# Optimization experiments

Measured on AMD Instinct MI355X. Metric: run time of the kernel, lower is better.

The kernel has to match this reference:

```python
import jax, jax.numpy as jnp
import numpy as np
import itertools

B, K, H, W = 64, 5, 320, 320
EPS = 1e-6
# All K! permutations (exact equivalent of scipy.linear_sum_assignment for KxK cost)
PERMS = np.array(list(itertools.permutations(range(K))), dtype=np.int32)  # [P, K]


def setup_inputs() -> dict:
    key = jax.random.key(0)
    k1, k2, k3 = jax.random.split(key, 3)
    return {
        "fg_logits": jax.random.normal(k1, (B, 1, H, W), dtype=jnp.float32),
        "slot_logits": jax.random.normal(k2, (B, K, H, W), dtype=jnp.float32),
        "target": jax.random.uniform(k3, (B, 1, H, W), dtype=jnp.float32),
    }


def reference(fg_logits, slot_logits, target):
    fg = target[:, 0]            # [B,H,W]
    bg = 1.0 - fg                # [B,H,W]
    # targets_b: index 0 = FG mask, 1..K-1 = BG mask (duplicated)  -> [B,K,H,W]
    targets = jnp.concatenate([fg[:, None], jnp.broadcast_to(bg[:, None], (B, K - 1, H, W))], axis=1)

    # IoU cost matrix on detached sigmoid probs (matches .detach())
    probs = jax.lax.stop_gradient(jax.nn.sigmoid(slot_logits))
    s = probs.reshape(B, K, -1)        # [B,K,N]
    t = targets.reshape(B, K, -1)      # [B,K,N]
    inter = jnp.einsum('bkn,bjn->bkj', s, t)           # [B,K,K]
    union = s.sum(-1)[:, :, None] + t.sum(-1)[:, None, :] - inter + EPS
    cost = 1.0 - inter / union                          # [B,K,K]

    # Exact Hungarian via brute force over K! permutations (K small)
    perms = jnp.asarray(PERMS)                          # [P,K]
    rows = jnp.arange(K)[None, :]                       # [1,K]
    perm_cost = cost[:, rows, perms].sum(-1)            # [B,P]
    best_perm = perms[jnp.argmin(perm_cost, axis=1)]    # [B,K] col_ind per sample

    # aligned[i] = targets[col_ind[i]]; targets[j] is fg iff j == 0
    is_fg = (best_perm == 0)[:, :, None, None]          # [B,K,1,1]
    aligned = jnp.where(is_fg, fg[:, None], bg[:, None])  # [B,K,H,W]

    # Stable sigmoid-BCE with logits, mean-reduced per sample then averaged over B
    x = slot_logits
    bce = jnp.maximum(x, 0.0) - x * aligned + jnp.log1p(jnp.exp(-jnp.abs(x)))
    return bce.mean()
```

## Files before the change

kernel.cpp:

```cpp
#include <hip/hip_runtime.h>


#define BB 64
#define KK 5
#define NPIX 102400
#define QUARTERS 4
#define SEG 25600
#define ITERS 25
#define THREADS 256
#define REC 8
#define NBLK (BB * KK * QUARTERS)

typedef float v4f __attribute__((ext_vector_type(4)));

__global__ void hung_pass1(const float* __restrict__ slot,
                           const float* __restrict__ tgt,
                           float* __restrict__ ws)
{
    const int bid = blockIdx.x;
    const int vid = (bid & 7) * (NBLK / 8) + (bid >> 3);
    const int q   = vid & (QUARTERS - 1);
    const int bk  = vid >> 2;
    const int b   = bk / KK;

    const float* xk = slot + (size_t)bk * NPIX + q * SEG;
    const float* t  = tgt  + (size_t)b  * NPIX + q * SEG;

    float X = 0.f, XF = 0.f, S = 0.f, SF = 0.f, PX = 0.f, Tf = 0.f;

    const int base = threadIdx.x * 4;
    #pragma unroll 5
    for (int i = 0; i < ITERS; ++i) {
        const int off = base + i * (THREADS * 4);
        const v4f fg4 = *reinterpret_cast<const v4f*>(t  + off);
        const v4f x4  = *reinterpret_cast<const v4f*>(xk + off);
        #pragma unroll
        for (int u = 0; u < 4; ++u) {
            const float x  = x4[u];
            const float fg = fg4[u];
            const float e  = __expf(-fabsf(x));
            const float qq = 1.0f + e;
            const float r  = __builtin_amdgcn_rcpf(qq);
            const float d  = __logf(qq) + fmaxf(-x, 0.0f);
            const float s  = (x >= 0.0f) ? r : e * r;
            PX += d;
            X  += x;
            XF  = fmaf(x, fg, XF);
            S  += s;
            SF  = fmaf(s, fg, SF);
            Tf += fg;
        }
    }

    float v[6] = {X, XF, S, SF, PX, Tf};
    #pragma unroll
    for (int j = 0; j < 6; ++j) {
        float x = v[j];
        #pragma unroll
        for (int off = 32; off > 0; off >>= 1) x += __shfl_down(x, off, 64);
        v[j] = x;
    }
    __shared__ float red[THREADS / 64][6];
    const int lane = threadIdx.x & 63;
    const int w    = threadIdx.x >> 6;
    if (lane == 0) {
        #pragma unroll
        for (int j = 0; j < 6; ++j) red[w][j] = v[j];
    }
    __syncthreads();
    if (threadIdx.x < 6) {
        const int j = threadIdx.x;
        ws[(size_t)vid * REC + j] =
            red[0][j] + red[1][j] + red[2][j] + red[3][j];
    }
}

__global__ __launch_bounds__(320) void hung_pass2(const float* __restrict__ ws,
                                                  float* __restrict__ out)
{
    __shared__ float red[BB][KK][6];
    const int t = threadIdx.x;
    if (t < BB * KK) {
        float v[6] = {0, 0, 0, 0, 0, 0};
        #pragma unroll
        for (int q = 0; q < QUARTERS; ++q) {
            const float* p = ws + (size_t)(t * QUARTERS + q) * REC;
            #pragma unroll
            for (int j = 0; j < 6; ++j) v[j] += p[j];
        }
        const int b = t / KK, k = t - b * KK;
        #pragma unroll
        for (int j = 0; j < 6; ++j) red[b][k][j] = v[j];
    }
    __syncthreads();
    if (t < BB) {
        const int b = t;
        const float Tf = red[b][0][5];
        const float Tb = (float)NPIX - Tf;
        float best = 3.402823466e+38f; int kb = 0;
        float xfsum = 0.f, px = 0.f;
        #pragma unroll
        for (int k = 0; k < KK; ++k) {
            const float Sv = red[b][k][2], Iv = red[b][k][3];
            const float cf = 1.f - Iv / (Sv + Tf - Iv + 1e-6f);
            const float Ib = Sv - Iv;
            const float cb = 1.f - Ib / (Sv + Tb - Ib + 1e-6f);
            const float dd = cf - cb;
            if (dd < best) { best = dd; kb = k; }
            xfsum += red[b][k][1];
            px    += red[b][k][4];
        }
        float res = px + xfsum - (2.f * red[b][kb][1] - red[b][kb][0]);
        #pragma unroll
        for (int off = 32; off > 0; off >>= 1) res += __shfl_down(res, off, 64);
        if (b == 0) out[0] = res * (1.0f / 32768000.0f);
    }
}

extern "C" void kernel_launch(void* const* d_in, const int* in_sizes, int n_in,
                              void* d_out, int out_size, void* d_ws, size_t ws_size,
                              hipStream_t stream) {
    const float* slot = (const float*)d_in[1];
    const float* tgt  = (const float*)d_in[2];
    float* out = (float*)d_out;
    float* ws  = (float*)d_ws;

    hung_pass1<<<NBLK, THREADS, 0, stream>>>(slot, tgt, ws);
    hung_pass2<<<1, 320, 0, stream>>>(ws, out);
}
```

Before: 223.1 us.

## Process all slots per block to reuse target loads across K

Restructures pass1 so each block covers one batch sample's pixel span for all K slots instead of one slot quarter. The target tile is loaded once and reused for all five slot channels, cutting redundant target reads. The cost is more accumulator registers and a larger per-block record (22 values), with pass2 adapted to reduce 20 partials per sample. The loop is no longer unrolled, which may reduce memory-level parallelism.

```diff
diff --git a/kernel.cpp b/kernel.cpp
--- a/kernel.cpp
+++ b/kernel.cpp
@@ -4,12 +4,12 @@
 #define BB 64
 #define KK 5
 #define NPIX 102400
-#define QUARTERS 4
-#define SEG 25600
-#define ITERS 25
+#define PB 20
+#define SPAN 5120
+#define ITERS 5
 #define THREADS 256
-#define REC 8
-#define NBLK (BB * KK * QUARTERS)
+#define REC 24
+#define NBLK (BB * PB)
 
 typedef float v4f __attribute__((ext_vector_type(4)));
 
@@ -18,99 +18,108 @@
                            float* __restrict__ ws)
 {
     const int bid = blockIdx.x;
-    const int vid = (bid & 7) * (NBLK / 8) + (bid >> 3);
-    const int q   = vid & (QUARTERS - 1);
-    const int bk  = vid >> 2;
-    const int b   = bk / KK;
+    const int b   = bid / PB;
+    const int pb  = bid - b * PB;
 
-    const float* xk = slot + (size_t)bk * NPIX + q * SEG;
-    const float* t  = tgt  + (size_t)b  * NPIX + q * SEG;
+    const float* t  = tgt  + (size_t)b * NPIX + pb * SPAN;
+    const float* xb = slot + (size_t)b * KK * NPIX + pb * SPAN;
 
-    float X = 0.f, XF = 0.f, S = 0.f, SF = 0.f, PX = 0.f, Tf = 0.f;
+    float X[KK]  = {0,0,0,0,0};
+    float XF[KK] = {0,0,0,0,0};
+    float S[KK]  = {0,0,0,0,0};
+    float SF[KK] = {0,0,0,0,0};
+    float PX = 0.f, Tf = 0.f;
 
-    const int base = threadIdx.x * 4;
-    #pragma unroll 5
+    const int tid4 = threadIdx.x * 4;
+    #pragma unroll 1
     for (int i = 0; i < ITERS; ++i) {
-        const int off = base + i * (THREADS * 4);
-        const v4f fg4 = *reinterpret_cast<const v4f*>(t  + off);
-        const v4f x4  = *reinterpret_cast<const v4f*>(xk + off);
+        const int off = tid4 + i * (THREADS * 4);
+        const v4f fg4 = *reinterpret_cast<const v4f*>(t + off);
         #pragma unroll
-        for (int u = 0; u < 4; ++u) {
-            const float x  = x4[u];
-            const float fg = fg4[u];
-            const float e  = __expf(-fabsf(x));
-            const float qq = 1.0f + e;
-            const float r  = __builtin_amdgcn_rcpf(qq);
-            const float d  = __logf(qq) + fmaxf(-x, 0.0f);
-            const float s  = (x >= 0.0f) ? r : e * r;
-            PX += d;
-            X  += x;
-            XF  = fmaf(x, fg, XF);
-            S  += s;
-            SF  = fmaf(s, fg, SF);
-            Tf += fg;
+        for (int k = 0; k < KK; ++k) {
+            const v4f x4 = *reinterpret_cast<const v4f*>(xb + (size_t)k * NPIX + off);
+            #pragma unroll
+            for (int u = 0; u < 4; ++u) {
+                const float x  = x4[u];
+                const float fg = fg4[u];
+                const float e  = __expf(-fabsf(x));
+                const float qq = 1.0f + e;
+                const float r  = __builtin_amdgcn_rcpf(qq);
+                const float d  = __logf(qq) + fmaxf(-x, 0.0f);
+                const float s  = (x >= 0.0f) ? r : e * r;
+                PX   += d;
+                X[k] += x;
+                XF[k] = fmaf(x, fg, XF[k]);
+                S[k] += s;
+                SF[k] = fmaf(s, fg, SF[k]);
+            }
         }
+        Tf += (fg4.x + fg4.y) + (fg4.z + fg4.w);
     }
 
-    float v[6] = {X, XF, S, SF, PX, Tf};
+    float v[22];
     #pragma unroll
-    for (int j = 0; j < 6; ++j) {
+    for (int k = 0; k < KK; ++k) {
+        v[k]      = X[k];
+        v[5 + k]  = XF[k];
+        v[10 + k] = S[k];
+        v[15 + k] = SF[k];
+    }
+    v[20] = PX;
+    v[21] = Tf;
+    #pragma unroll
+    for (int j = 0; j < 22; ++j) {
         float x = v[j];
         #pragma unroll
         for (int off = 32; off > 0; off >>= 1) x += __shfl_down(x, off, 64);
         v[j] = x;
     }
-    __shared__ float red[THREADS / 64][6];
+    __shared__ float red[THREADS / 64][22];
     const int lane = threadIdx.x & 63;
     const int w    = threadIdx.x >> 6;
     if (lane == 0) {
         #pragma unroll
-        for (int j = 0; j < 6; ++j) red[w][j] = v[j];
+        for (int j = 0; j < 22; ++j) red[w][j] = v[j];
     }
     __syncthreads();
-    if (threadIdx.x < 6) {
+    if (threadIdx.x < 22) {
         const int j = threadIdx.x;
-        ws[(size_t)vid * REC + j] =
+        ws[(size_t)bid * REC + j] =
             red[0][j] + red[1][j] + red[2][j] + red[3][j];
     }
 }
 
-__global__ __launch_bounds__(320) void hung_pass2(const float* __restrict__ ws,
+__global__ __launch_bounds__(256) void hung_pass2(const float* __restrict__ ws,
                                                   float* __restrict__ out)
 {
-    __shared__ float red[BB][KK][6];
-    const int t = threadIdx.x;
-    if (t < BB * KK) {
-        float v[6] = {0, 0, 0, 0, 0, 0};
-        #pragma unroll
-        for (int q = 0; q < QUARTERS; ++q) {
-            const float* p = ws + (size_t)(t * QUARTERS + q) * REC;
-            #pragma unroll
-            for (int j = 0; j < 6; ++j) v[j] += p[j];
-        }
-        const int b = t / KK, k = t - b * KK;
-        #pragma unroll
-        for (int j = 0; j < 6; ++j) red[b][k][j] = v[j];
+    __shared__ float red[BB][22];
+    for (int idx = threadIdx.x; idx < BB * 22; idx += 256) {
+        const int b = idx / 22, j = idx - b * 22;
+        float s = 0.f;
+        #pragma unroll 4
+        for (int pb = 0; pb < PB; ++pb)
+            s += ws[(size_t)(b * PB + pb) * REC + j];
+        red[b][j] = s;
     }
     __syncthreads();
-    if (t < BB) {
-        const int b = t;
-        const float Tf = red[b][0][5];
+    if (threadIdx.x < 64) {
+        const int b = threadIdx.x;
+        const float* v = red[b];
+        const float Tf = v[21];
         const float Tb = (float)NPIX - Tf;
         float best = 3.402823466e+38f; int kb = 0;
-        float xfsum = 0.f, px = 0.f;
+        float xfsum = 0.f;
         #pragma unroll
         for (int k = 0; k < KK; ++k) {
-            const float Sv = red[b][k][2], Iv = red[b][k][3];
+            const float Sv = v[10 + k], Iv = v[15 + k];
             const float cf = 1.f - Iv / (Sv + Tf - Iv + 1e-6f);
             const float Ib = Sv - Iv;
             const float cb = 1.f - Ib / (Sv + Tb - Ib + 1e-6f);
             const float dd = cf - cb;
             if (dd < best) { best = dd; kb = k; }
-            xfsum += red[b][k][1];
-            px    += red[b][k][4];
+            xfsum += v[5 + k];
         }
-        float res = px + xfsum - (2.f * red[b][kb][1] - red[b][kb][0]);
+        float res = v[20] + xfsum - (2.f * v[5 + kb] - v[kb]);
         #pragma unroll
         for (int off = 32; off > 0; off >>= 1) res += __shfl_down(res, off, 64);
         if (b == 0) out[0] = res * (1.0f / 32768000.0f);
@@ -126,5 +135,5 @@
     float* ws  = (float*)d_ws;
 
     hung_pass1<<<NBLK, THREADS, 0, stream>>>(slot, tgt, ws);
-    hung_pass2<<<1, 320, 0, stream>>>(ws, out);
+    hung_pass2<<<1, 256, 0, stream>>>(ws, out);
 }
```

Result: slower. 236.4 us (+6.0%).
